# Kernel optimization log

Hardware: AMD Instinct MI355X
Metric: run time of the kernel (lower is better)

Reference implementation:

```python
import jax, jax.numpy as jnp
import numpy as np

EPS = 1e-5
CONV_CFG = [(10, 5, 3), (8, 5, 2), (4, 2, 1), (3, 1, 1), (3, 1, 1)]  # (kernel, stride, pad)


def conv_bn_relu(x, w, gamma, beta, stride, pad):
    # x: [B, Cin, L], w: [Cout, Cin, K]; BatchNorm1d in training mode (batch stats)
    y = jax.lax.conv_general_dilated(x, w, (stride,), [(pad, pad)],
                                     dimension_numbers=('NCH', 'OIH', 'NCH'))
    mean = y.mean(axis=(0, 2), keepdims=True)
    var = y.var(axis=(0, 2), keepdims=True)
    y = (y - mean) * jax.lax.rsqrt(var + EPS)
    return jax.nn.relu(y * gamma[None, :, None] + beta[None, :, None])


def encoder(x, ws, bn_gamma, bn_beta):
    for i, (k, s, p) in enumerate(CONV_CFG):
        x = conv_bn_relu(x, ws[i], bn_gamma[i], bn_beta[i], s, p)
    return x


def gru(seq, h0, wih, whh, bih, bhh):
    # seq: [B, T, D], h0: [B, H]. torch GRU gate order: r, z, n.
    x_proj = jnp.einsum('btd,gd->btg', seq, wih) + bih  # [B, T, 3H]

    def step(h, xp):
        hp = h @ whh.T + bhh
        xr, xz, xn = jnp.split(xp, 3, axis=-1)
        hr, hz, hn = jnp.split(hp, 3, axis=-1)
        r = jax.nn.sigmoid(xr + hr)
        zg = jax.nn.sigmoid(xz + hz)
        n = jnp.tanh(xn + r * hn)
        h_new = (1.0 - zg) * n + zg * h
        return h_new, h_new

    h_last, outs = jax.lax.scan(step, h0, jnp.swapaxes(x_proj, 0, 1))
    return jnp.swapaxes(outs, 0, 1), h_last


def setup_inputs() -> dict:
    key = jax.random.key(0)
    ks = jax.random.split(key, 16)
    B, L, T = 64, 20480, 12
    x = jax.random.normal(ks[0], (B, 1, L), dtype=jnp.float32)
    hidden = jnp.zeros((1, B, 256), dtype=jnp.float32)
    shapes = [(512, 1, 10), (512, 512, 8), (512, 512, 4), (512, 512, 3), (512, 512, 3)]
    ws = {}
    for i, sh in enumerate(shapes):
        fan_out = sh[0] * sh[2]
        ws['w%d' % (i + 1)] = jax.random.normal(ks[1 + i], sh, dtype=jnp.float32) * np.float32(np.sqrt(2.0 / fan_out))
    bn_gamma = jnp.ones((5, 512), dtype=jnp.float32)
    bn_beta = jnp.zeros((5, 512), dtype=jnp.float32)
    gru_wih = jax.random.normal(ks[6], (768, 512), dtype=jnp.float32) * np.float32(np.sqrt(2.0 / 768.0))
    gru_whh = jax.random.normal(ks[7], (768, 256), dtype=jnp.float32) * np.float32(np.sqrt(2.0 / 768.0))
    gru_bih = jnp.zeros((768,), dtype=jnp.float32)
    gru_bhh = jnp.zeros((768,), dtype=jnp.float32)
    wk_w = jax.random.normal(ks[8], (T, 512, 256), dtype=jnp.float32) * np.float32(np.sqrt(2.0 / 512.0))
    wk_b = jnp.zeros((T, 512), dtype=jnp.float32)
    inp = dict(x=x, hidden=hidden, bn_gamma=bn_gamma, bn_beta=bn_beta,
               gru_wih=gru_wih, gru_whh=gru_whh, gru_bih=gru_bih, gru_bhh=gru_bhh,
               wk_w=wk_w, wk_b=wk_b, t_samples=200)
    inp.update(ws)
    return inp


def reference(x, hidden, w1, w2, w3, w4, w5, bn_gamma, bn_beta,
              gru_wih, gru_whh, gru_bih, gru_bhh, wk_w, wk_b, t_samples):
    B = x.shape[0]
    T = wk_w.shape[0]
    t = int(t_samples)
    z = encoder(x, (w1, w2, w3, w4, w5), bn_gamma, bn_beta)  # [B, 512, Lz]
    z = jnp.swapaxes(z, 1, 2)                                # [B, Lz, 512]
    encode_samples = jnp.swapaxes(z[:, t + 1:t + 1 + T, :], 0, 1)  # [T, B, 512]
    forward_seq = z[:, :t + 1, :]
    output, h_last = gru(forward_seq, hidden[0], gru_wih, gru_whh, gru_bih, gru_bhh)
    c_t = output[:, t, :]                                    # [B, 256]
    pred = jnp.einsum('bd,tkd->tbk', c_t, wk_w) + wk_b[:, None, :]  # [T, B, 512]
    total = jnp.einsum('tbk,tck->tbc', encode_samples, pred)        # [T, B, B]
    logsm = jax.nn.log_softmax(total, axis=-1)  # nn.LogSoftmax() on 2D -> dim=1
    nce = jnp.sum(jnp.diagonal(logsm, axis1=1, axis2=2)) / (-1.0 * B * T)
    # torch overwrites `correct` each iteration -> final value is from the last timestep
    correct = jnp.sum(jnp.argmax(jax.nn.softmax(total[-1], axis=-1), axis=0) == jnp.arange(B))
    accuracy = correct.astype(jnp.float32) / B
    return accuracy, nce, h_last[None]
```

## Files before the change

### kernel.cpp

```cpp
#include <hip/hip_runtime.h>
#include <hip/hip_bf16.h>

typedef __hip_bfloat16 bf16;
typedef short short8v __attribute__((ext_vector_type(8)));
typedef float float4v __attribute__((ext_vector_type(4)));

__device__ __forceinline__ float ld_f(const float* p, size_t i) { return p[i]; }
__device__ __forceinline__ float ld_f(const bf16* p, size_t i) { return __bfloat162float(p[i]); }
__device__ __forceinline__ float bfb_to_f(short u) {
    return __uint_as_float(((unsigned int)(unsigned short)u) << 16);
}
__device__ __forceinline__ short f_to_bf16bits(float v) {
    bf16 h = __float2bfloat16(v);
    short s; __builtin_memcpy(&s, &h, 2); return s;
}
__device__ __forceinline__ unsigned int bn_pair(unsigned int u, float sc, float sh) {
    float x0 = bfb_to_f((short)(u & 0xffffu));
    float x1 = bfb_to_f((short)(u >> 16));
    float y0 = fmaxf(fmaf(sc, x0, sh), 0.0f);
    float y1 = fmaxf(fmaf(sc, x1, sh), 0.0f);
    return (unsigned int)(unsigned short)f_to_bf16bits(y0) |
           ((unsigned int)(unsigned short)f_to_bf16bits(y1) << 16);
}
__device__ __forceinline__ float sigmoidf_(float x) { return 1.0f / (1.0f + expf(-x)); }

__global__ __launch_bounds__(256) void zero_kernel(float* __restrict__ p, int n) {
    int i = blockIdx.x * 256 + threadIdx.x;
    if (i < n) p[i] = 0.0f;
}

__global__ __launch_bounds__(256) void pack_gemm(const float* __restrict__ w, short* __restrict__ out,
                                                 int M, int CIN, int KW, int KWP) {
    int idx = blockIdx.x * 256 + threadIdx.x;
    int tot = M * CIN * KWP;
    if (idx >= tot) return;
    int co = idx / (CIN * KWP);
    int r = idx - co * (CIN * KWP);
    int ci = r / KWP, t = r - ci * KWP;
    float v = (t < KW) ? w[((size_t)co * CIN + ci) * KW + t] : 0.0f;
    out[idx] = f_to_bf16bits(v);
}

__global__ __launch_bounds__(256) void pack_gruw(const float* __restrict__ whh, short* __restrict__ wfrag) {
    int idx = blockIdx.x * 256 + threadIdx.x;
    if (idx >= 196608) return;
    int j = idx & 7;
    int lane = (idx >> 3) & 63;
    int f = idx >> 9;
    int wv = f / 48;
    int r = f - wv * 48;
    int mt = r >> 3, kc = r & 7;
    int m = lane & 15, quad = lane >> 4;
    int row = (wv * 6 + mt) * 16 + m;
    int col = kc * 32 + quad * 8 + j;
    wfrag[idx] = f_to_bf16bits(whh[(size_t)row * 256 + col]);
}

__global__ __launch_bounds__(256) void pack_all(const float* __restrict__ w3, const float* __restrict__ w4,
                                                const float* __restrict__ w5, const float* __restrict__ wih,
                                                const float* __restrict__ whh,
                                                short* __restrict__ o3, short* __restrict__ o4,
                                                short* __restrict__ o5, short* __restrict__ owih,
                                                short* __restrict__ ogru) {
    int idx = blockIdx.x * 256 + threadIdx.x;
    const int NC = 512 * 512 * 4;
    if (idx < NC) {
        int co = idx >> 11, r = idx & 2047;
        int ci = r >> 2, t = r & 3;
        o3[idx] = f_to_bf16bits(w3[((size_t)co * 512 + ci) * 4 + t]);
        return;
    }
    idx -= NC;
    if (idx < NC) {
        int co = idx >> 11, r = idx & 2047;
        int ci = r >> 2, t = r & 3;
        o4[idx] = (t < 3) ? f_to_bf16bits(w4[((size_t)co * 512 + ci) * 3 + t]) : 0;
        return;
    }
    idx -= NC;
    if (idx < NC) {
        int co = idx >> 11, r = idx & 2047;
        int ci = r >> 2, t = r & 3;
        o5[idx] = (t < 3) ? f_to_bf16bits(w5[((size_t)co * 512 + ci) * 3 + t]) : 0;
        return;
    }
    idx -= NC;
    if (idx < 393216) {
        owih[idx] = f_to_bf16bits(wih[idx]);
        return;
    }
    idx -= 393216;
    if (idx < 196608) {
        int j = idx & 7;
        int lane = (idx >> 3) & 63;
        int f = idx >> 9;
        int wv = f / 48;
        int r = f - wv * 48;
        int mt = r >> 3, kc = r & 7;
        int m = lane & 15, quad = lane >> 4;
        int row = (wv * 6 + mt) * 16 + m;
        int col = kc * 32 + quad * 8 + j;
        ogru[idx] = f_to_bf16bits(whh[(size_t)row * 256 + col]);
    }
}

__global__ __launch_bounds__(256) void bn_fin(const float* __restrict__ sums, const float* __restrict__ gamma,
                                              const float* __restrict__ beta, int layer, float invM,
                                              float* __restrict__ ss) {
    int c = blockIdx.x * 256 + threadIdx.x;
    if (c >= 512) return;
    float mean = sums[c] * invM;
    float var = sums[512 + c] * invM - mean * mean;
    float sc = rsqrtf(var + 1e-5f) * gamma[layer * 512 + c];
    ss[c] = sc;
    ss[512 + c] = beta[layer * 512 + c] - mean * sc;
}

template <int KWP, int ST, int SPANP, bool BNIN, bool STATS>
__global__ __launch_bounds__(256, 3) void conv_mfma6(const bf16* __restrict__ in,
                                                     const short* __restrict__ wpk,
                                                     bf16* __restrict__ out,
                                                     int Lin, int Lout, int pad,
                                                     const float* __restrict__ ssin,
                                                     float* __restrict__ sums_out) {
    constexpr int KTOT = 512 * KWP;
    constexpr int NCHUNK = KTOT / 32;
    constexpr int CCC = 32 / KWP;
    constexpr int W16 = SPANP / 8;
    constexpr int NU = CCC * W16;
    constexpr int NLD = (NU + 255) / 256;

    const int l0 = blockIdx.x * 128;
    const int co0 = blockIdx.y * 128;
    const int tid = threadIdx.x;
    const int lane = tid & 63;
    const int wv = tid >> 6;
    const int m = lane & 15;
    const int quad = lane >> 4;
    const int nh = wv * 32;

    in += (size_t)blockIdx.z * 512 * Lin;
    out += (size_t)blockIdx.z * 512 * Lout;
    const short* ins = (const short*)in;

    __shared__ __align__(16) short As[2][128][40];
    __shared__ __align__(16) short rows[2][CCC][SPANP];
    __shared__ float bsum[STATS ? 128 : 1][2];

    const int base = ST * l0 - pad;
    const int g0a = base & ~7;
    const int off = base - g0a;

    const int arow = tid >> 2, aseg = tid & 3;

    float4v acc[8][2];
#pragma unroll
    for (int i = 0; i < 8; ++i) { acc[i][0] = (float4v){0,0,0,0}; acc[i][1] = (float4v){0,0,0,0}; }

    uint4 pa0, pa1;
    uint4 rbuf[NLD];

    auto load_stage = [&](int kc) {
        const int k0 = kc * 32;
        const int ci0 = kc * CCC;
        pa0 = *(const uint4*)(wpk + (size_t)(co0 + arow) * KTOT + k0 + aseg * 8);
        pa1 = *(const uint4*)(wpk + (size_t)(co0 + arow + 64) * KTOT + k0 + aseg * 8);
#pragma unroll
        for (int r = 0; r < NLD; ++r) {
            int e = tid + r * 256;
            if (NU % 256 == 0 || e < NU) {
                int cc = e / W16, col = e - cc * W16;
                int gs = g0a + col * 8;
                const short* src = ins + (size_t)(ci0 + cc) * Lin;
                if (gs >= 0 && gs + 8 <= Lin) {
                    rbuf[r] = *(const uint4*)(src + gs);
                } else {
                    float sc = 0.f, sh = 0.f;
                    if constexpr (BNIN) { sc = ssin[ci0 + cc]; sh = ssin[512 + ci0 + cc]; }
                    unsigned short tmp[8];
#pragma unroll
                    for (int j = 0; j < 8; ++j) {
                        int g = gs + j;
                        float xv = 0.f;
                        if (g >= 0 && g < Lin) {
                            xv = bfb_to_f(src[g]);
                            if constexpr (BNIN) xv = fmaxf(fmaf(sc, xv, sh), 0.0f);
                        }
                        tmp[j] = (unsigned short)f_to_bf16bits(xv);
                    }
                    uint4 v;
                    v.x = tmp[0] | ((unsigned int)tmp[1] << 16);
                    v.y = tmp[2] | ((unsigned int)tmp[3] << 16);
                    v.z = tmp[4] | ((unsigned int)tmp[5] << 16);
                    v.w = tmp[6] | ((unsigned int)tmp[7] << 16);
                    rbuf[r] = v;
                }
            }
        }
    };
    auto commit = [&](int buf, int kc) {
        *(uint4*)&As[buf][arow][aseg * 8] = pa0;
        *(uint4*)&As[buf][arow + 64][aseg * 8] = pa1;
        const int ci0 = kc * CCC;
#pragma unroll
        for (int r = 0; r < NLD; ++r) {
            int e = tid + r * 256;
            if (NU % 256 == 0 || e < NU) {
                int cc = e / W16, col = e - cc * W16;
                uint4 v = rbuf[r];
                if constexpr (BNIN) {
                    int gs = g0a + col * 8;
                    if (gs >= 0 && gs + 8 <= Lin) {
                        float sc = ssin[ci0 + cc], sh = ssin[512 + ci0 + cc];
                        v.x = bn_pair(v.x, sc, sh);
                        v.y = bn_pair(v.y, sc, sh);
                        v.z = bn_pair(v.z, sc, sh);
                        v.w = bn_pair(v.w, sc, sh);
                    }
                }
                *(uint4*)&rows[buf][cc][col * 8] = v;
            }
        }
    };

    if (STATS && tid < 128) { bsum[tid][0] = 0.f; bsum[tid][1] = 0.f; }
    load_stage(0);
    commit(0, 0);
    __syncthreads();

    for (int kc = 0; kc < NCHUNK; ++kc) {
        const int cur = kc & 1;
        if (kc + 1 < NCHUNK) load_stage(kc + 1);

        short8v afrag[8], bfrag[2];
#pragma unroll
        for (int s = 0; s < 8; ++s)
            afrag[s] = *(const short8v*)&As[cur][s * 16 + m][quad * 8];
#pragma unroll
        for (int t = 0; t < 2; ++t) {
            const int ll = nh + t * 16 + m;
            short8v bf;
            if constexpr (KWP == 8) {
                const short* rp = &rows[cur][quad][off + ST * ll];
#pragma unroll
                for (int j = 0; j < 8; ++j) bf[j] = rp[j];
            } else {
                const short* ra = &rows[cur][quad * 2 + 0][off + ST * ll];
                const short* rb = &rows[cur][quad * 2 + 1][off + ST * ll];
#pragma unroll
                for (int j = 0; j < 4; ++j) { bf[j] = ra[j]; bf[4 + j] = rb[j]; }
            }
            bfrag[t] = bf;
        }
#pragma unroll
        for (int s = 0; s < 8; ++s)
#pragma unroll
            for (int t = 0; t < 2; ++t)
                acc[s][t] = __builtin_amdgcn_mfma_f32_16x16x32_bf16(afrag[s], bfrag[t], acc[s][t], 0, 0, 0);

        if (kc + 1 < NCHUNK) commit(cur ^ 1, kc + 1);
        __syncthreads();
    }

    const bool v0 = (l0 + nh + m) < Lout;
    const bool v1 = (l0 + nh + 16 + m) < Lout;
#pragma unroll
    for (int t = 0; t < 2; ++t) {
        const int l = l0 + nh + t * 16 + m;
        if (t ? v1 : v0) {
#pragma unroll
            for (int s = 0; s < 8; ++s) {
#pragma unroll
                for (int reg = 0; reg < 4; ++reg) {
                    const int co = co0 + s * 16 + quad * 4 + reg;
                    out[(size_t)co * Lout + l] = __float2bfloat16(acc[s][t][reg]);
                }
            }
        }
    }

    if constexpr (STATS) {
#pragma unroll
        for (int s = 0; s < 8; ++s) {
            float p1[4], p2[4];
#pragma unroll
            for (int reg = 0; reg < 4; ++reg) {
                float a0 = v0 ? acc[s][0][reg] : 0.f;
                float a1 = v1 ? acc[s][1][reg] : 0.f;
                p1[reg] = a0 + a1;
                p2[reg] = a0 * a0 + a1 * a1;
            }
#pragma unroll
            for (int o = 1; o <= 8; o <<= 1) {
#pragma unroll
                for (int reg = 0; reg < 4; ++reg) {
                    p1[reg] += __shfl_xor(p1[reg], o);
                    p2[reg] += __shfl_xor(p2[reg], o);
                }
            }
            if (m == 0) {
#pragma unroll
                for (int reg = 0; reg < 4; ++reg) {
                    atomicAdd(&bsum[s * 16 + quad * 4 + reg][0], p1[reg]);
                    atomicAdd(&bsum[s * 16 + quad * 4 + reg][1], p2[reg]);
                }
            }
        }
        __syncthreads();
        if (tid < 128) {
            atomicAdd(&sums_out[co0 + tid], bsum[tid][0]);
            atomicAdd(&sums_out[512 + co0 + tid], bsum[tid][1]);
        }
    }
}

template <int KWP, int ST, int SPANP, bool BNIN, bool STATS>
__global__ __launch_bounds__(256, 2) void conv_mfma7(const bf16* __restrict__ in,
                                                     const short* __restrict__ wpk,
                                                     bf16* __restrict__ out,
                                                     int Lin, int Lout, int pad,
                                                     const float* __restrict__ ssin,
                                                     float* __restrict__ sums_out) {
    constexpr int KTOT = 512 * KWP;
    constexpr int NCHUNK = KTOT / 32;
    constexpr int CCC = 32 / KWP;
    constexpr int W16 = SPANP / 8;
    constexpr int NU = CCC * W16;

    const int l0 = blockIdx.x * 64;
    const int tid = threadIdx.x;
    const int lane = tid & 63;
    const int wv = tid >> 6;
    const int m = lane & 15;
    const int quad = lane >> 4;
    const int ch = (wv >> 1) * 256;
    const int wl = (wv & 1) * 32;

    in += (size_t)blockIdx.y * 512 * Lin;
    out += (size_t)blockIdx.y * 512 * Lout;
    const short* ins = (const short*)in;

    __shared__ __align__(16) short As[2][512][32];
    __shared__ __align__(16) short rows[2][CCC][SPANP];
    __shared__ float bsum[STATS ? 512 : 1][2];

    const int base = ST * l0 - pad;
    const int g0a = base & ~7;
    const int off = base - g0a;

    const int aco = tid >> 2, aseg = tid & 3;

    float4v acc[16][2];
#pragma unroll
    for (int i = 0; i < 16; ++i) { acc[i][0] = (float4v){0,0,0,0}; acc[i][1] = (float4v){0,0,0,0}; }

    uint4 pa[8];
    uint4 rb;

    auto load_stage = [&](int kc) {
        const int k0 = kc * 32;
        const int ci0 = kc * CCC;
#pragma unroll
        for (int r = 0; r < 8; ++r)
            pa[r] = *(const uint4*)(wpk + (size_t)(aco + r * 64) * KTOT + k0 + aseg * 8);
        if (tid < NU) {
            int cc = tid / W16, col = tid - cc * W16;
            int gs = g0a + col * 8;
            const short* src = ins + (size_t)(ci0 + cc) * Lin;
            if (gs >= 0 && gs + 8 <= Lin) {
                rb = *(const uint4*)(src + gs);
            } else {
                float sc = 0.f, sh = 0.f;
                if constexpr (BNIN) { sc = ssin[ci0 + cc]; sh = ssin[512 + ci0 + cc]; }
                unsigned short tmp[8];
#pragma unroll
                for (int j = 0; j < 8; ++j) {
                    int g = gs + j;
                    float xv = 0.f;
                    if (g >= 0 && g < Lin) {
                        xv = bfb_to_f(src[g]);
                        if constexpr (BNIN) xv = fmaxf(fmaf(sc, xv, sh), 0.0f);
                    }
                    tmp[j] = (unsigned short)f_to_bf16bits(xv);
                }
                uint4 v;
                v.x = tmp[0] | ((unsigned int)tmp[1] << 16);
                v.y = tmp[2] | ((unsigned int)tmp[3] << 16);
                v.z = tmp[4] | ((unsigned int)tmp[5] << 16);
                v.w = tmp[6] | ((unsigned int)tmp[7] << 16);
                rb = v;
            }
        }
    };
    auto commit = [&](int buf, int kc) {
#pragma unroll
        for (int r = 0; r < 8; ++r)
            *(uint4*)&As[buf][aco + r * 64][aseg * 8] = pa[r];
        if (tid < NU) {
            int cc = tid / W16, col = tid - cc * W16;
            uint4 v = rb;
            if constexpr (BNIN) {
                int gs = g0a + col * 8;
                if (gs >= 0 && gs + 8 <= Lin) {
                    const int ci0 = kc * CCC;
                    float sc = ssin[ci0 + cc], sh = ssin[512 + ci0 + cc];
                    v.x = bn_pair(v.x, sc, sh);
                    v.y = bn_pair(v.y, sc, sh);
                    v.z = bn_pair(v.z, sc, sh);
                    v.w = bn_pair(v.w, sc, sh);
                }
            }
            *(uint4*)&rows[buf][cc][col * 8] = v;
        }
    };

    if (STATS) {
        for (int i = tid; i < 512; i += 256) { bsum[i][0] = 0.f; bsum[i][1] = 0.f; }
    }
    load_stage(0);
    commit(0, 0);
    __syncthreads();

    for (int kc = 0; kc < NCHUNK; ++kc) {
        const int cur = kc & 1;
        if (kc + 1 < NCHUNK) load_stage(kc + 1);

        short8v bfrag[2];
#pragma unroll
        for (int t = 0; t < 2; ++t) {
            const int ll = wl + t * 16 + m;
            short8v bf;
            if constexpr (KWP == 8) {
                const short* rp = &rows[cur][quad][off + ST * ll];
#pragma unroll
                for (int j = 0; j < 8; ++j) bf[j] = rp[j];
            } else {
                const short* ra = &rows[cur][quad * 2 + 0][off + ST * ll];
                const short* rb2 = &rows[cur][quad * 2 + 1][off + ST * ll];
#pragma unroll
                for (int j = 0; j < 4; ++j) { bf[j] = ra[j]; bf[4 + j] = rb2[j]; }
            }
            bfrag[t] = bf;
        }
#pragma unroll
        for (int s = 0; s < 16; ++s) {
            short8v afrag = *(const short8v*)&As[cur][ch + s * 16 + m][quad * 8];
            acc[s][0] = __builtin_amdgcn_mfma_f32_16x16x32_bf16(afrag, bfrag[0], acc[s][0], 0, 0, 0);
            acc[s][1] = __builtin_amdgcn_mfma_f32_16x16x32_bf16(afrag, bfrag[1], acc[s][1], 0, 0, 0);
        }

        if (kc + 1 < NCHUNK) commit(cur ^ 1, kc + 1);
        __syncthreads();
    }

    const bool v0 = (l0 + wl + m) < Lout;
    const bool v1 = (l0 + wl + 16 + m) < Lout;
#pragma unroll
    for (int t = 0; t < 2; ++t) {
        const int l = l0 + wl + t * 16 + m;
        if (t ? v1 : v0) {
#pragma unroll
            for (int s = 0; s < 16; ++s) {
#pragma unroll
                for (int reg = 0; reg < 4; ++reg) {
                    const int co = ch + s * 16 + quad * 4 + reg;
                    out[(size_t)co * Lout + l] = __float2bfloat16(acc[s][t][reg]);
                }
            }
        }
    }

    if constexpr (STATS) {
#pragma unroll
        for (int s = 0; s < 16; ++s) {
            float p1[4], p2[4];
#pragma unroll
            for (int reg = 0; reg < 4; ++reg) {
                float a0 = v0 ? acc[s][0][reg] : 0.f;
                float a1 = v1 ? acc[s][1][reg] : 0.f;
                p1[reg] = a0 + a1;
                p2[reg] = a0 * a0 + a1 * a1;
            }
#pragma unroll
            for (int o = 1; o <= 8; o <<= 1) {
#pragma unroll
                for (int reg = 0; reg < 4; ++reg) {
                    p1[reg] += __shfl_xor(p1[reg], o);
                    p2[reg] += __shfl_xor(p2[reg], o);
                }
            }
            if (m == 0) {
#pragma unroll
                for (int reg = 0; reg < 4; ++reg) {
                    atomicAdd(&bsum[ch + s * 16 + quad * 4 + reg][0], p1[reg]);
                    atomicAdd(&bsum[ch + s * 16 + quad * 4 + reg][1], p2[reg]);
                }
            }
        }
        __syncthreads();
        for (int i = tid; i < 512; i += 256) {
            atomicAdd(&sums_out[i], bsum[i][0]);
            atomicAdd(&sums_out[512 + i], bsum[i][1]);
        }
    }
}

__global__ __launch_bounds__(256) void conv1_mfma(const float* __restrict__ x,
                                                  const short* __restrict__ w1p,
                                                  const float* __restrict__ ss,
                                                  bf16* __restrict__ y1c, int nbase) {
    const int l0 = blockIdx.x * 64;
    const int co0 = blockIdx.y * 128;
    const int nloc = blockIdx.z;
    const int n = nbase + nloc;
    const int tid = threadIdx.x;
    const int lane = tid & 63;
    const int wv = tid >> 6;
    const int m = lane & 15;
    const int quad = lane >> 4;

    __shared__ __align__(16) short xs[352];
    const int base = 5 * l0 - 3;
    for (int e = tid; e < 347; e += 256) {
        int g = base + e;
        float v = (g >= 0 && g < 20480) ? x[(size_t)n * 20480 + g] : 0.0f;
        xs[e] = f_to_bf16bits(v);
    }
    __syncthreads();

    const int lloc = wv * 16 + m;
    short8v bfrag;
    {
        const short* rp = &xs[5 * lloc + quad * 8];
#pragma unroll
        for (int j = 0; j < 8; ++j) bfrag[j] = rp[j];
    }
    float4v acc[8];
#pragma unroll
    for (int s = 0; s < 8; ++s) {
        short8v afrag = *(const short8v*)(w1p + (size_t)(co0 + s * 16 + m) * 32 + quad * 8);
        float4v z = (float4v){0.f, 0.f, 0.f, 0.f};
        acc[s] = __builtin_amdgcn_mfma_f32_16x16x32_bf16(afrag, bfrag, z, 0, 0, 0);
    }
    const int l = l0 + lloc;
#pragma unroll
    for (int s = 0; s < 8; ++s) {
#pragma unroll
        for (int reg = 0; reg < 4; ++reg) {
            const int co = co0 + s * 16 + quad * 4 + reg;
            float v = fmaxf(acc[s][reg] * ss[co] + ss[512 + co], 0.0f);
            y1c[((size_t)nloc * 512 + co) * 4096 + l] = __float2bfloat16(v);
        }
    }
}

__global__ __launch_bounds__(256) void conv1_stats(const float* __restrict__ x,
                                                   const float* __restrict__ w1,
                                                   float* __restrict__ sums) {
    const int n = blockIdx.x;
    const int tid = threadIdx.x;
    __shared__ __align__(16) float ws[5120];
    __shared__ __align__(16) float xs[5 * 256 + 10];
    for (int e = tid; e < 5120; e += 256) ws[e] = w1[e];
    const int co0 = tid, co1 = tid + 256;
    float a1_0 = 0.0f, a2_0 = 0.0f, a1_1 = 0.0f, a2_1 = 0.0f;
    for (int i = 0; i < 4; ++i) {
        const int c = blockIdx.y * 4 + i;
        const int base = c * 1280 - 3;
        __syncthreads();
        for (int e = tid; e < 1290; e += 256) {
            int g = base + e;
            xs[e] = (g >= 0 && g < 20480) ? x[(size_t)n * 20480 + g] : 0.0f;
        }
        __syncthreads();
        for (int l = 0; l < 256; ++l) {
            float y0 = 0.0f, y1v = 0.0f;
#pragma unroll
            for (int t = 0; t < 10; ++t) {
                float xv = xs[5 * l + t];
                y0 += ws[co0 * 10 + t] * xv;
                y1v += ws[co1 * 10 + t] * xv;
            }
            a1_0 += y0; a2_0 += y0 * y0;
            a1_1 += y1v; a2_1 += y1v * y1v;
        }
    }
    atomicAdd(&sums[co0], a1_0); atomicAdd(&sums[512 + co0], a2_0);
    atomicAdd(&sums[co1], a1_1); atomicAdd(&sums[512 + co1], a2_1);
}

__global__ __launch_bounds__(256) void bn_stats_v(const bf16* __restrict__ y, float* __restrict__ sums, int L) {
    const int c = blockIdx.x, n = blockIdx.y;
    const short* p = (const short*)y + ((size_t)n * 512 + c) * L;
    float s1 = 0.f, s2 = 0.f;
    for (int l = threadIdx.x; l < L; l += 256) {
        float v = bfb_to_f(p[l]);
        s1 += v; s2 += v * v;
    }
#pragma unroll
    for (int off = 32; off > 0; off >>= 1) {
        s1 += __shfl_down(s1, off, 64);
        s2 += __shfl_down(s2, off, 64);
    }
    __shared__ float r1[4], r2[4];
    const int lane = threadIdx.x & 63, wv = threadIdx.x >> 6;
    if (lane == 0) { r1[wv] = s1; r2[wv] = s2; }
    __syncthreads();
    if (threadIdx.x == 0) {
        atomicAdd(&sums[c], r1[0] + r1[1] + r1[2] + r1[3]);
        atomicAdd(&sums[512 + c], r2[0] + r2[1] + r2[2] + r2[3]);
    }
}

__global__ __launch_bounds__(256) void bn_apply_v(bf16* __restrict__ y, const float* __restrict__ sums,
                                                  const float* __restrict__ gamma, const float* __restrict__ beta,
                                                  int layer, int L) {
    const int c = blockIdx.x, n = blockIdx.y;
    const float invM = 1.0f / (64.0f * (float)L);
    float mean = sums[c] * invM;
    float var = sums[512 + c] * invM - mean * mean;
    float sc = rsqrtf(var + 1e-5f) * gamma[layer * 512 + c];
    float sh = beta[layer * 512 + c] - mean * sc;
    short* p = (short*)y + ((size_t)n * 512 + c) * L;
    for (int l = threadIdx.x; l < L; l += 256) {
        float v = bfb_to_f(p[l]);
        p[l] = f_to_bf16bits(fmaxf(v * sc + sh, 0.0f));
    }
}

__global__ __launch_bounds__(256) void xproj_mfma(const bf16* __restrict__ y5,
                                                  const short* __restrict__ wihp,
                                                  const float* __restrict__ bih,
                                                  const float* __restrict__ ssy,
                                                  float* __restrict__ xp,
                                                  const int* __restrict__ tsamp) {
    const int t0 = blockIdx.x * 64;
    const int g0 = blockIdx.y * 128;
    const int b = blockIdx.z;
    const int tid = threadIdx.x;
    const int lane = tid & 63;
    const int wv = tid >> 6;
    const int m = lane & 15;
    const int quad = lane >> 4;
    const int ts = tsamp[0];

    __shared__ __align__(16) short As[128][40];
    __shared__ __align__(16) short Bt[32][66];

    float4v acc[8];
#pragma unroll
    for (int i = 0; i < 8; ++i) acc[i] = (float4v){0.f, 0.f, 0.f, 0.f};

    const short* y5s = (const short*)y5;
    for (int kc = 0; kc < 16; ++kc) {
        const int k0 = kc * 32;
        __syncthreads();
#pragma unroll
        for (int r = 0; r < 2; ++r) {
            int e = tid + r * 256;
            int row = e >> 2, seg = e & 3;
            *(uint4*)&As[row][seg * 8] =
                *(const uint4*)(wihp + (size_t)(g0 + row) * 512 + k0 + seg * 8);
        }
        for (int e = tid; e < 2048; e += 256) {
            int cc = e >> 6, tl = e & 63;
            float sc = ssy[k0 + cc], sh = ssy[512 + k0 + cc];
            float xv = bfb_to_f(y5s[((size_t)b * 512 + k0 + cc) * 409 + t0 + tl]);
            Bt[cc][tl] = f_to_bf16bits(fmaxf(fmaf(sc, xv, sh), 0.0f));
        }
        __syncthreads();
        short8v bfrag;
#pragma unroll
        for (int j = 0; j < 8; ++j) bfrag[j] = Bt[quad * 8 + j][wv * 16 + m];
#pragma unroll
        for (int s = 0; s < 8; ++s) {
            short8v afrag = *(const short8v*)&As[s * 16 + m][quad * 8];
            acc[s] = __builtin_amdgcn_mfma_f32_16x16x32_bf16(afrag, bfrag, acc[s], 0, 0, 0);
        }
    }
    const int t = t0 + wv * 16 + m;
    if (t <= ts) {
#pragma unroll
        for (int s = 0; s < 8; ++s) {
#pragma unroll
            for (int reg = 0; reg < 4; ++reg) {
                const int g = g0 + s * 16 + quad * 4 + reg;
                xp[((size_t)b * 256 + t) * 768 + g] = acc[s][reg] + bih[g];
            }
        }
    }
}

__global__ __launch_bounds__(512, 2) void gru_mfma(const float* __restrict__ xproj,
                                                   const short* __restrict__ wfrag,
                                                   const float* __restrict__ hidden,
                                                   const float* __restrict__ bhh,
                                                   float* __restrict__ hlast,
                                                   const int* __restrict__ tsamp) {
    const int b = blockIdx.x;
    const int tid = threadIdx.x;
    const int lane = tid & 63;
    const int wv = tid >> 6;
    const int m = lane & 15;
    const int quad = lane >> 4;

    __shared__ float hf[256];
    __shared__ __align__(16) short hbs[256];
    __shared__ float pre[768];

    short8v wreg[48];
    {
        const short* wb = wfrag + ((size_t)(wv * 48) * 64 + lane) * 8;
#pragma unroll
        for (int f = 0; f < 48; ++f) wreg[f] = *(const short8v*)(wb + (size_t)f * 512);
    }
    if (wv < 4) {
        float hv = hidden[(size_t)b * 256 + tid];
        hf[tid] = hv;
        hbs[tid] = f_to_bf16bits(hv);
    }
    const int ts = tsamp[0];
    const float* xb = xproj + (size_t)b * 256 * 768;
    float bhr = 0.f, bhz = 0.f, bhn = 0.f, nxr = 0.f, nxz = 0.f, nxn = 0.f;
    if (wv < 4) {
        bhr = bhh[tid]; bhz = bhh[256 + tid]; bhn = bhh[512 + tid];
        nxr = xb[tid]; nxz = xb[256 + tid]; nxn = xb[512 + tid];
    }

    for (int step = 0; step <= ts; ++step) {
        __syncthreads();
        float4v acc[6];
#pragma unroll
        for (int i = 0; i < 6; ++i) acc[i] = (float4v){0.f, 0.f, 0.f, 0.f};
#pragma unroll
        for (int kc = 0; kc < 8; ++kc) {
            short8v bfrag = *(const short8v*)&hbs[kc * 32 + quad * 8];
#pragma unroll
            for (int mt = 0; mt < 6; ++mt)
                acc[mt] = __builtin_amdgcn_mfma_f32_16x16x32_bf16(wreg[mt * 8 + kc], bfrag, acc[mt], 0, 0, 0);
        }
        if (m == 0) {
#pragma unroll
            for (int mt = 0; mt < 6; ++mt)
#pragma unroll
                for (int reg = 0; reg < 4; ++reg)
                    pre[wv * 96 + mt * 16 + quad * 4 + reg] = acc[mt][reg];
        }
        __syncthreads();
        if (wv < 4) {
            const int g = tid;
            float r = sigmoidf_(nxr + bhr + pre[g]);
            float z = sigmoidf_(nxz + bhz + pre[256 + g]);
            float nn = tanhf(nxn + r * (bhn + pre[512 + g]));
            float hnew = (1.0f - z) * nn + z * hf[g];
            hf[g] = hnew;
            hbs[g] = f_to_bf16bits(hnew);
            if (step < ts) {
                const float* xs = xb + (size_t)(step + 1) * 768;
                nxr = xs[g]; nxz = xs[256 + g]; nxn = xs[512 + g];
            }
        }
    }
    __syncthreads();
    if (wv < 4) hlast[(size_t)b * 256 + tid] = hf[tid];
}

__global__ __launch_bounds__(256) void pred_kernel(const float* __restrict__ hlast, const float* __restrict__ wkw,
                                                   const float* __restrict__ wkb, float* __restrict__ pred) {
    const int c = blockIdx.x, t = blockIdx.y;
    __shared__ __align__(16) float hs[256];
    hs[threadIdx.x] = hlast[(size_t)c * 256 + threadIdx.x];
    __syncthreads();
    for (int k = threadIdx.x; k < 512; k += 256) {
        const float* wr = wkw + ((size_t)t * 512 + k) * 256;
        float acc = 0.0f;
        for (int d = 0; d < 256; d += 4) {
            float4 w4 = *(const float4*)&wr[d];
            acc += w4.x * hs[d] + w4.y * hs[d + 1] + w4.z * hs[d + 2] + w4.w * hs[d + 3];
        }
        pred[((size_t)t * 64 + c) * 512 + k] = acc + wkb[(size_t)t * 512 + k];
    }
}

__global__ __launch_bounds__(64) void total_kernel(const bf16* __restrict__ y5, const float* __restrict__ pred,
                                                   const float* __restrict__ ssy,
                                                   float* __restrict__ total, const int* __restrict__ tsamp) {
    const int b = blockIdx.x, t = blockIdx.y;
    const int col = tsamp[0] + 1 + t;
    __shared__ __align__(16) float es[512];
    for (int k = threadIdx.x; k < 512; k += 64) {
        float xv = ld_f(y5, ((size_t)b * 512 + k) * 409 + col);
        es[k] = fmaxf(fmaf(ssy[k], xv, ssy[512 + k]), 0.0f);
    }
    __syncthreads();
    const int c = threadIdx.x;
    const float* pr = pred + ((size_t)t * 64 + c) * 512;
    float acc = 0.0f;
    for (int k = 0; k < 512; k += 4) {
        float4 p4 = *(const float4*)&pr[k];
        acc += p4.x * es[k] + p4.y * es[k + 1] + p4.z * es[k + 2] + p4.w * es[k + 3];
    }
    total[((size_t)t * 64 + b) * 64 + c] = acc;
}

__global__ __launch_bounds__(256) void final_kernel(const float* __restrict__ total, const float* __restrict__ hlast,
                                                    float* __restrict__ out) {
    __shared__ float rowM[768], rowS[768];
    __shared__ float red[256];
    __shared__ int cnt[64];
    const int tid = threadIdx.x;
    float local = 0.0f;
    for (int row = tid; row < 768; row += 256) {
        const float* r = total + (size_t)row * 64;
        float m = r[0];
        for (int c = 1; c < 64; ++c) m = fmaxf(m, r[c]);
        float s = 0.0f;
        for (int c = 0; c < 64; ++c) s += expf(r[c] - m);
        rowM[row] = m; rowS[row] = s;
        int bcol = row & 63;
        local += r[bcol] - m - logf(s);
    }
    red[tid] = local;
    __syncthreads();
    for (int o = 128; o > 0; o >>= 1) {
        if (tid < o) red[tid] += red[tid + o];
        __syncthreads();
    }
    if (tid == 0) out[1] = red[0] / (-768.0f);
    if (tid < 64) {
        const int c = tid;
        float best = -1e30f; int bi = -1;
        for (int b = 0; b < 64; ++b) {
            int row = 11 * 64 + b;
            float v = expf(total[(size_t)row * 64 + c] - rowM[row]) / rowS[row];
            if (v > best) { best = v; bi = b; }
        }
        cnt[c] = (bi == c) ? 1 : 0;
    }
    __syncthreads();
    if (tid == 0) {
        int s = 0;
        for (int c = 0; c < 64; ++c) s += cnt[c];
        out[0] = (float)s / 64.0f;
    }
    for (int i = tid; i < 16384; i += 256) out[2 + i] = hlast[i];
}

extern "C" void kernel_launch(void* const* d_in, const int* in_sizes, int n_in,
                              void* d_out, int out_size, void* d_ws, size_t ws_size,
                              hipStream_t stream) {
    const float *x = nullptr, *hidden = nullptr, *gamma = nullptr, *beta = nullptr;
    const float *wih = nullptr, *whh = nullptr, *bih = nullptr, *bhh = nullptr;
    const float *wkw = nullptr, *wkb = nullptr;
    const float *w1 = nullptr, *w2 = nullptr, *w3 = nullptr, *w4 = nullptr, *w5 = nullptr;
    const int* tsamp = nullptr;
    for (int i = 0; i < n_in; ++i) {
        const float* p = (const float*)d_in[i];
        switch (in_sizes[i]) {
            case 1310720: x = p; break;
            case 16384:   hidden = p; break;
            case 2560:    if (!gamma) gamma = p; else beta = p; break;
            case 393216:  wih = p; break;
            case 196608:  whh = p; break;
            case 768:     if (!bih) bih = p; else bhh = p; break;
            case 1572864: wkw = p; break;
            case 6144:    wkb = p; break;
            case 1:       tsamp = (const int*)d_in[i]; break;
            case 5120:    w1 = p; break;
            case 2097152: w2 = p; break;
            case 1048576: w3 = p; break;
            case 786432:  if (!w4) w4 = p; else w5 = p; break;
            default: break;
        }
    }

    char* ws = (char*)d_ws;
    const size_t SLOT_B = 57872384ull;
    int NBC = 8;
    if (ws_size >= SLOT_B + 64ull * 4194304ull + 98304ull) NBC = 64;
    else if (ws_size >= SLOT_B + 32ull * 4194304ull + 98304ull) NBC = 32;
    else if (ws_size >= SLOT_B + 16ull * 4194304ull + 98304ull) NBC = 16;

    bf16*  y2    = (bf16*)(ws + 0);
    bf16*  y4    = (bf16*)(ws + 0);
    float* xp    = (float*)(ws + 0);
    short* wconv = (short*)(ws + 53676032ull);
    bf16*  y1c   = (bf16*)(ws + SLOT_B);
    bf16*  y3    = (bf16*)(ws + SLOT_B);
    bf16*  y5    = (bf16*)(ws + SLOT_B);
    const size_t tail = SLOT_B + (size_t)NBC * 4194304ull;
    float* sums  = (float*)(ws + tail);
    float* ss1   = (float*)(ws + tail + 20480ull);
    float* ss2   = (float*)(ws + tail + 24576ull);
    float* ss3   = (float*)(ws + tail + 28672ull);
    float* ss4   = (float*)(ws + tail + 32768ull);
    float* ss5   = (float*)(ws + tail + 36864ull);
    short* w1p   = (short*)(ws + tail + 40960ull);

    float* hlast = (float*)(ws + 54855680ull);
    float* pred  = (float*)(ws + 54921216ull);
    float* totl  = (float*)(ws + 56494080ull);

    short *wpk3, *wpk4, *wpk5, *wihp, *wfrag;
    if (NBC == 64) {
        wpk3  = (short*)(ws + SLOT_B + 33554432ull);
        wpk4  = wpk3 + 1048576;
        wpk5  = wpk4 + 1048576;
        wihp  = wpk5 + 1048576;
        wfrag = wihp + 393216;
    } else {
        wpk3 = wpk4 = wpk5 = wconv;
        wihp  = (short*)(ws + 53676032ull);
        wfrag = (short*)(ws + 54462464ull);
    }

    zero_kernel<<<20, 256, 0, stream>>>(sums, 5120);
    conv1_stats<<<dim3(64, 4), 256, 0, stream>>>(x, w1, sums);
    bn1_finalize_launch:
    bn_fin<<<2, 256, 0, stream>>>(sums, gamma, beta, 0, 1.0f / (64.0f * 4096.0f), ss1);
    pack_gemm<<<64, 256, 0, stream>>>(w1, w1p, 512, 1, 10, 32);
    pack_gemm<<<8192, 256, 0, stream>>>(w2, wconv, 512, 512, 8, 8);

    if (NBC == 64) {
        conv1_mfma<<<dim3(64, 4, 64), 256, 0, stream>>>(x, w1p, ss1, y1c, 0);
        conv_mfma6<8, 5, 656, false, true><<<dim3(7, 4, 64), 256, 0, stream>>>(
            y1c, wconv, y2, 4096, 819, 2, nullptr, sums + 1024);
        pack_all<<<14592, 256, 0, stream>>>(w3, w4, w5, wih, whh, wpk3, wpk4, wpk5, wihp, wfrag);
        bn_fin<<<2, 256, 0, stream>>>(sums + 1024, gamma, beta, 1, 1.0f / (64.0f * 819.0f), ss2);

        conv_mfma7<4, 2, 144, true, true><<<dim3(7, 64), 256, 0, stream>>>(
            y2, wpk3, y3, 819, 409, 1, ss2, sums + 2048);
        bn_fin<<<2, 256, 0, stream>>>(sums + 2048, gamma, beta, 2, 1.0f / (64.0f * 409.0f), ss3);

        conv_mfma7<4, 1, 80, true, true><<<dim3(7, 64), 256, 0, stream>>>(
            y3, wpk4, y4, 409, 409, 1, ss3, sums + 3072);
        bn_fin<<<2, 256, 0, stream>>>(sums + 3072, gamma, beta, 3, 1.0f / (64.0f * 409.0f), ss4);

        conv_mfma7<4, 1, 80, true, true><<<dim3(7, 64), 256, 0, stream>>>(
            y4, wpk5, y5, 409, 409, 1, ss4, sums + 4096);
        bn_fin<<<2, 256, 0, stream>>>(sums + 4096, gamma, beta, 4, 1.0f / (64.0f * 409.0f), ss5);
    } else {
        for (int nb = 0; nb < 64; nb += NBC) {
            conv1_mfma<<<dim3(64, 4, NBC), 256, 0, stream>>>(x, w1p, ss1, y1c, nb);
            conv_mfma6<8, 5, 656, false, false><<<dim3(7, 4, NBC), 256, 0, stream>>>(
                y1c, wconv, y2 + (size_t)nb * 512 * 819, 4096, 819, 2, nullptr, nullptr);
        }
        bn_stats_v<<<dim3(512, 64), 256, 0, stream>>>(y2, sums + 1024, 819);
        bn_apply_v<<<dim3(512, 64), 256, 0, stream>>>(y2, sums + 1024, gamma, beta, 1, 819);

        pack_gemm<<<4096, 256, 0, stream>>>(w3, wconv, 512, 512, 4, 4);
        conv_mfma7<4, 2, 144, false, false><<<dim3(7, 64), 256, 0, stream>>>(
            y2, wconv, y3, 819, 409, 1, nullptr, nullptr);
        bn_stats_v<<<dim3(512, 64), 256, 0, stream>>>(y3, sums + 2048, 409);
        bn_apply_v<<<dim3(512, 64), 256, 0, stream>>>(y3, sums + 2048, gamma, beta, 2, 409);

        pack_gemm<<<4096, 256, 0, stream>>>(w4, wconv, 512, 512, 3, 4);
        conv_mfma7<4, 1, 80, false, false><<<dim3(7, 64), 256, 0, stream>>>(
            y3, wconv, y4, 409, 409, 1, nullptr, nullptr);
        bn_stats_v<<<dim3(512, 64), 256, 0, stream>>>(y4, sums + 3072, 409);
        bn_apply_v<<<dim3(512, 64), 256, 0, stream>>>(y4, sums + 3072, gamma, beta, 3, 409);

        pack_gemm<<<4096, 256, 0, stream>>>(w5, wconv, 512, 512, 3, 4);
        conv_mfma7<4, 1, 80, false, false><<<dim3(7, 64), 256, 0, stream>>>(
            y4, wconv, y5, 409, 409, 1, nullptr, nullptr);
        bn_stats_v<<<dim3(512, 64), 256, 0, stream>>>(y5, sums + 4096, 409);
        bn_fin<<<2, 256, 0, stream>>>(sums + 4096, gamma, beta, 4, 1.0f / (64.0f * 409.0f), ss5);

        pack_gemm<<<1536, 256, 0, stream>>>(wih, wihp, 768, 512, 1, 1);
        pack_gruw<<<768, 256, 0, stream>>>(whh, wfrag);
    }

    xproj_mfma<<<dim3(4, 6, 64), 256, 0, stream>>>(y5, wihp, bih, ss5, xp, tsamp);
    gru_mfma<<<64, 512, 0, stream>>>(xp, wfrag, hidden, bhh, hlast, tsamp);

    pred_kernel<<<dim3(64, 12), 256, 0, stream>>>(hlast, wkw, wkb, pred);
    total_kernel<<<dim3(64, 12), 64, 0, stream>>>(y5, pred, ss5, totl, tsamp);
    final_kernel<<<1, 256, 0, stream>>>(totl, hlast, (float*)d_out);
}
```

Before: 2.528 ms.

## Split conv3-5 output channels across two blocks with padded LDS and higher occupancy

New measurement: 2.598 ms. 2.8% more time.

```diff
diff --git a/kernel.cpp b/kernel.cpp
--- a/kernel.cpp
+++ b/kernel.cpp
@@ -315,7 +315,7 @@
 }
 
 template <int KWP, int ST, int SPANP, bool BNIN, bool STATS>
-__global__ __launch_bounds__(256, 2) void conv_mfma7(const bf16* __restrict__ in,
+__global__ __launch_bounds__(256, 3) void conv_mfma8(const bf16* __restrict__ in,
                                                      const short* __restrict__ wpk,
                                                      bf16* __restrict__ out,
                                                      int Lin, int Lout, int pad,
@@ -328,41 +328,42 @@
     constexpr int NU = CCC * W16;
 
     const int l0 = blockIdx.x * 64;
+    const int co0 = blockIdx.y * 256;
     const int tid = threadIdx.x;
     const int lane = tid & 63;
     const int wv = tid >> 6;
     const int m = lane & 15;
     const int quad = lane >> 4;
-    const int ch = (wv >> 1) * 256;
+    const int ch = (wv >> 1) * 128;
     const int wl = (wv & 1) * 32;
 
-    in += (size_t)blockIdx.y * 512 * Lin;
-    out += (size_t)blockIdx.y * 512 * Lout;
+    in += (size_t)blockIdx.z * 512 * Lin;
+    out += (size_t)blockIdx.z * 512 * Lout;
     const short* ins = (const short*)in;
 
-    __shared__ __align__(16) short As[2][512][32];
+    __shared__ __align__(16) short As[2][256][40];
     __shared__ __align__(16) short rows[2][CCC][SPANP];
-    __shared__ float bsum[STATS ? 512 : 1][2];
+    __shared__ float bsum[STATS ? 256 : 1][2];
 
     const int base = ST * l0 - pad;
     const int g0a = base & ~7;
     const int off = base - g0a;
 
-    const int aco = tid >> 2, aseg = tid & 3;
-
-    float4v acc[16][2];
-#pragma unroll
-    for (int i = 0; i < 16; ++i) { acc[i][0] = (float4v){0,0,0,0}; acc[i][1] = (float4v){0,0,0,0}; }
-
-    uint4 pa[8];
+    const int arow = tid >> 2, aseg = tid & 3;
+
+    float4v acc[8][2];
+#pragma unroll
+    for (int i = 0; i < 8; ++i) { acc[i][0] = (float4v){0,0,0,0}; acc[i][1] = (float4v){0,0,0,0}; }
+
+    uint4 pa[4];
     uint4 rb;
 
     auto load_stage = [&](int kc) {
         const int k0 = kc * 32;
         const int ci0 = kc * CCC;
 #pragma unroll
-        for (int r = 0; r < 8; ++r)
-            pa[r] = *(const uint4*)(wpk + (size_t)(aco + r * 64) * KTOT + k0 + aseg * 8);
+        for (int r = 0; r < 4; ++r)
+            pa[r] = *(const uint4*)(wpk + (size_t)(co0 + arow + r * 64) * KTOT + k0 + aseg * 8);
         if (tid < NU) {
             int cc = tid / W16, col = tid - cc * W16;
             int gs = g0a + col * 8;
@@ -394,8 +395,8 @@
     };
     auto commit = [&](int buf, int kc) {
 #pragma unroll
-        for (int r = 0; r < 8; ++r)
-            *(uint4*)&As[buf][aco + r * 64][aseg * 8] = pa[r];
+        for (int r = 0; r < 4; ++r)
+            *(uint4*)&As[buf][arow + r * 64][aseg * 8] = pa[r];
         if (tid < NU) {
             int cc = tid / W16, col = tid - cc * W16;
             uint4 v = rb;
@@ -414,9 +415,7 @@
         }
     };
 
-    if (STATS) {
-        for (int i = tid; i < 512; i += 256) { bsum[i][0] = 0.f; bsum[i][1] = 0.f; }
-    }
+    if (STATS) { bsum[tid][0] = 0.f; bsum[tid][1] = 0.f; }
     load_stage(0);
     commit(0, 0);
     __syncthreads();
@@ -425,7 +424,10 @@
         const int cur = kc & 1;
         if (kc + 1 < NCHUNK) load_stage(kc + 1);
 
-        short8v bfrag[2];
+        short8v afrag[8], bfrag[2];
+#pragma unroll
+        for (int s = 0; s < 8; ++s)
+            afrag[s] = *(const short8v*)&As[cur][ch + s * 16 + m][quad * 8];
 #pragma unroll
         for (int t = 0; t < 2; ++t) {
             const int ll = wl + t * 16 + m;
@@ -443,11 +445,10 @@
             bfrag[t] = bf;
         }
 #pragma unroll
-        for (int s = 0; s < 16; ++s) {
-            short8v afrag = *(const short8v*)&As[cur][ch + s * 16 + m][quad * 8];
-            acc[s][0] = __builtin_amdgcn_mfma_f32_16x16x32_bf16(afrag, bfrag[0], acc[s][0], 0, 0, 0);
-            acc[s][1] = __builtin_amdgcn_mfma_f32_16x16x32_bf16(afrag, bfrag[1], acc[s][1], 0, 0, 0);
-        }
+        for (int s = 0; s < 8; ++s)
+#pragma unroll
+            for (int t = 0; t < 2; ++t)
+                acc[s][t] = __builtin_amdgcn_mfma_f32_16x16x32_bf16(afrag[s], bfrag[t], acc[s][t], 0, 0, 0);
 
         if (kc + 1 < NCHUNK) commit(cur ^ 1, kc + 1);
         __syncthreads();
@@ -460,10 +461,10 @@
         const int l = l0 + wl + t * 16 + m;
         if (t ? v1 : v0) {
 #pragma unroll
-            for (int s = 0; s < 16; ++s) {
+            for (int s = 0; s < 8; ++s) {
 #pragma unroll
                 for (int reg = 0; reg < 4; ++reg) {
-                    const int co = ch + s * 16 + quad * 4 + reg;
+                    const int co = co0 + ch + s * 16 + quad * 4 + reg;
                     out[(size_t)co * Lout + l] = __float2bfloat16(acc[s][t][reg]);
                 }
             }
@@ -472,7 +473,7 @@
 
     if constexpr (STATS) {
 #pragma unroll
-        for (int s = 0; s < 16; ++s) {
+        for (int s = 0; s < 8; ++s) {
             float p1[4], p2[4];
 #pragma unroll
             for (int reg = 0; reg < 4; ++reg) {
@@ -498,10 +499,8 @@
             }
         }
         __syncthreads();
-        for (int i = tid; i < 512; i += 256) {
-            atomicAdd(&sums_out[i], bsum[i][0]);
-            atomicAdd(&sums_out[512 + i], bsum[i][1]);
-        }
+        atomicAdd(&sums_out[co0 + tid], bsum[tid][0]);
+        atomicAdd(&sums_out[512 + co0 + tid], bsum[tid][1]);
     }
 }
 
@@ -916,7 +915,6 @@
 
     zero_kernel<<<20, 256, 0, stream>>>(sums, 5120);
     conv1_stats<<<dim3(64, 4), 256, 0, stream>>>(x, w1, sums);
-    bn1_finalize_launch:
     bn_fin<<<2, 256, 0, stream>>>(sums, gamma, beta, 0, 1.0f / (64.0f * 4096.0f), ss1);
     pack_gemm<<<64, 256, 0, stream>>>(w1, w1p, 512, 1, 10, 32);
     pack_gemm<<<8192, 256, 0, stream>>>(w2, wconv, 512, 512, 8, 8);
@@ -928,15 +926,15 @@
         pack_all<<<14592, 256, 0, stream>>>(w3, w4, w5, wih, whh, wpk3, wpk4, wpk5, wihp, wfrag);
         bn_fin<<<2, 256, 0, stream>>>(sums + 1024, gamma, beta, 1, 1.0f / (64.0f * 819.0f), ss2);
 
-        conv_mfma7<4, 2, 144, true, true><<<dim3(7, 64), 256, 0, stream>>>(
+        conv_mfma8<4, 2, 144, true, true><<<dim3(7, 2, 64), 256, 0, stream>>>(
             y2, wpk3, y3, 819, 409, 1, ss2, sums + 2048);
         bn_fin<<<2, 256, 0, stream>>>(sums + 2048, gamma, beta, 2, 1.0f / (64.0f * 409.0f), ss3);
 
-        conv_mfma7<4, 1, 80, true, true><<<dim3(7, 64), 256, 0, stream>>>(
+        conv_mfma8<4, 1, 80, true, true><<<dim3(7, 2, 64), 256, 0, stream>>>(
             y3, wpk4, y4, 409, 409, 1, ss3, sums + 3072);
         bn_fin<<<2, 256, 0, stream>>>(sums + 3072, gamma, beta, 3, 1.0f / (64.0f * 409.0f), ss4);
 
-        conv_mfma7<4, 1, 80, true, true><<<dim3(7, 64), 256, 0, stream>>>(
+        conv_mfma8<4, 1, 80, true, true><<<dim3(7, 2, 64), 256, 0, stream>>>(
             y4, wpk5, y5, 409, 409, 1, ss4, sums + 4096);
         bn_fin<<<2, 256, 0, stream>>>(sums + 4096, gamma, beta, 4, 1.0f / (64.0f * 409.0f), ss5);
     } else {
@@ -949,19 +947,19 @@
         bn_apply_v<<<dim3(512, 64), 256, 0, stream>>>(y2, sums + 1024, gamma, beta, 1, 819);
 
         pack_gemm<<<4096, 256, 0, stream>>>(w3, wconv, 512, 512, 4, 4);
-        conv_mfma7<4, 2, 144, false, false><<<dim3(7, 64), 256, 0, stream>>>(
+        conv_mfma8<4, 2, 144, false, false><<<dim3(7, 2, 64), 256, 0, stream>>>(
             y2, wconv, y3, 819, 409, 1, nullptr, nullptr);
         bn_stats_v<<<dim3(512, 64), 256, 0, stream>>>(y3, sums + 2048, 409);
         bn_apply_v<<<dim3(512, 64), 256, 0, stream>>>(y3, sums + 2048, gamma, beta, 2, 409);
 
         pack_gemm<<<4096, 256, 0, stream>>>(w4, wconv, 512, 512, 3, 4);
-        conv_mfma7<4, 1, 80, false, false><<<dim3(7, 64), 256, 0, stream>>>(
+        conv_mfma8<4, 1, 80, false, false><<<dim3(7, 2, 64), 256, 0, stream>>>(
             y3, wconv, y4, 409, 409, 1, nullptr, nullptr);
         bn_stats_v<<<dim3(512, 64), 256, 0, stream>>>(y4, sums + 3072, 409);
         bn_apply_v<<<dim3(512, 64), 256, 0, stream>>>(y4, sums + 3072, gamma, beta, 3, 409);
 
         pack_gemm<<<4096, 256, 0, stream>>>(w5, wconv, 512, 512, 3, 4);
-        conv_mfma7<4, 1, 80, false, false><<<dim3(7, 64), 256, 0, stream>>>(
+        conv_mfma8<4, 1, 80, false, false><<<dim3(7, 2, 64), 256, 0, stream>>>(
             y4, wconv, y5, 409, 409, 1, nullptr, nullptr);
         bn_stats_v<<<dim3(512, 64), 256, 0, stream>>>(y5, sums + 4096, 409);
         bn_fin<<<2, 256, 0, stream>>>(sums + 4096, gamma, beta, 4, 1.0f / (64.0f * 409.0f), ss5);
```
